# Optimization experiments

Hardware: AMD Instinct MI355X
Metric: run time of the kernel (lower is better)

The kernel has to match this reference:

```python
import jax, jax.numpy as jnp
import numpy as np

BNH, L, D = 32, 1024, 64        # (b*nh, seq_len, d_k)
CLIP = 64                        # rel_pos_clip
R = 2 * CLIP + 1                 # rel-pos table rows = 129
TEMP = 8.0                       # temperature = sqrt(d_k)


def setup_inputs() -> dict:
    key = jax.random.key(0)
    ks = jax.random.split(key, 7)
    q = jax.random.normal(ks[0], (BNH, L, D), jnp.float32)
    k = jax.random.normal(ks[1], (BNH, L, D), jnp.float32)
    v = jax.random.normal(ks[2], (BNH, L, D), jnp.float32)
    attn_w = jax.random.normal(ks[3], (BNH, L, L), jnp.float32)
    emb_k = jax.random.normal(ks[4], (R, D), jnp.float32)
    emb_v = jax.random.normal(ks[5], (R, D), jnp.float32)
    pos_seqs = jnp.sort(jax.random.randint(ks[6], (BNH, L), 0, 2048), axis=-1)
    mask = jnp.zeros((BNH, L, L), dtype=bool)  # no positions masked
    return {"q": q, "k": k, "v": v, "attn_w": attn_w,
            "emb_k": emb_k, "emb_v": emb_v,
            "pos_seqs": pos_seqs, "mask": mask}


def reference(q, k, v, attn_w, emb_k, emb_v, pos_seqs, mask):
    # relative-position index table: table[b,j,k] = clip(pos[k]-pos[j]) + CLIP, in [0, 2*CLIP]
    table = jnp.clip(pos_seqs[:, None, :] - pos_seqs[:, :, None], -CLIP, CLIP) + CLIP  # (bnh,l,l)

    # content scores
    attn = jnp.einsum('bid,bjd->bij', q, k)  # (bnh,l,l)

    # rel-pos key term: einsum('ijm,ijkm->ijk', q, emb_k[table]) done WITHOUT
    # materializing the (bnh,l,l,d) gather: project q onto all R embeddings,
    # then gather along the R axis (same math, far less memory traffic).
    qe = jnp.einsum('bid,rd->bir', q, emb_k)                 # (bnh,l,R)
    attn = attn + jnp.take_along_axis(qe, table, axis=2)     # (bnh,l,l)

    # score_util == 'np': additive posterior scores
    attn = attn + attn_w

    attn = attn / TEMP
    attn = jnp.where(mask, -jnp.inf, attn)
    p = jax.nn.softmax(attn, axis=2)
    # dropout is identity in eval mode

    out = jnp.einsum('bij,bjd->bid', p, v)                   # (bnh,l,d)

    # rel-pos value term: einsum('ijk,ijkm->ijm', p, emb_v[table]) via
    # scatter-add of probs into R buckets, then one small GEMM.
    bi = jnp.arange(BNH)[:, None, None]
    li = jnp.arange(L)[None, :, None]
    av = jnp.zeros((BNH, L, R), p.dtype).at[bi, li, table].add(p)  # (bnh,l,R)
    out = out + jnp.einsum('bir,rd->bid', av, emb_v)
    return out, p
```

## Files before the change

kernel.cpp:

```cpp
#include <hip/hip_runtime.h>
#include <hip/hip_bf16.h>

#define BNH 32
#define L 1024
#define D 64
#define RP 129
#define CLIPV 64
#define TI 16
#define TJ 256
#define NT 256

typedef __attribute__((ext_vector_type(8))) short bf16x8;
typedef __attribute__((ext_vector_type(4))) float f32x4;

__device__ __forceinline__ unsigned short f2bf(float f) {
    unsigned int u = __builtin_bit_cast(unsigned int, f);
    return (unsigned short)((u + 0x7fffu + ((u >> 16) & 1u)) >> 16);
}

__global__ __launch_bounds__(NT) void qe_kernel(const float* __restrict__ q,
                                                const float* __restrict__ emb_k,
                                                float* __restrict__ p_out) {
    __shared__ float e_s[RP][68];
    __shared__ float q_s[8][68];
    const int tid = threadIdx.x;
    const int b = blockIdx.x >> 7;
    const int i0 = (blockIdx.x & 127) * 8;

    for (int t = tid; t < RP * 16; t += NT) {
        int r = t >> 4, c4 = t & 15;
        *reinterpret_cast<float4*>(&e_s[r][c4 * 4]) =
            *reinterpret_cast<const float4*>(emb_k + r * D + c4 * 4);
    }
    for (int t = tid; t < 8 * 16; t += NT) {
        int row = t >> 4, c4 = t & 15;
        *reinterpret_cast<float4*>(&q_s[row][c4 * 4]) =
            *reinterpret_cast<const float4*>(q + ((size_t)(b * L + i0 + row)) * D + c4 * 4);
    }
    __syncthreads();

    const int row = tid >> 5;
    const int rr = tid & 31;
    for (int r = rr; r < RP; r += 32) {
        float acc = 0.f;
#pragma unroll
        for (int d4 = 0; d4 < 16; ++d4) {
            float4 qv = *reinterpret_cast<const float4*>(&q_s[row][d4 * 4]);
            float4 ev = *reinterpret_cast<const float4*>(&e_s[r][d4 * 4]);
            acc += qv.x * ev.x + qv.y * ev.y + qv.z * ev.z + qv.w * ev.w;
        }
        p_out[((size_t)(b * L + i0 + row)) * L + r] = acc;
    }
}

__global__ __launch_bounds__(NT, 2) void attn_kernel(
    const float* __restrict__ q, const float* __restrict__ k, const float* __restrict__ v,
    const float* __restrict__ attn_w, const float* __restrict__ emb_v,
    const int* __restrict__ pos, const unsigned char* __restrict__ mask,
    float* __restrict__ out, float* __restrict__ p_out) {

    __shared__ __attribute__((aligned(16))) unsigned short kv_u[TJ * 72];
    __shared__ __attribute__((aligned(16))) unsigned short q_u[TI * 72];
    __shared__ unsigned short pos_s[L];
    __shared__ float qe_s[TI * RP];
    __shared__ float av_s[TI * RP];
    __shared__ float out_s[TI * 68];
    __shared__ float m_part[4][16];
    __shared__ float m_s[16];
    __shared__ float l_s[16];

    const int tid = threadIdx.x;
    const int b = blockIdx.x >> 6;
    const int i0 = (blockIdx.x & 63) * TI;
    const int w = tid >> 6;
    const int lane = tid & 63;
    const int quad = lane >> 4;
    const int lo = lane & 15;

    for (int t = tid; t < L; t += NT) pos_s[t] = (unsigned short)pos[b * L + t];
    if (tid < TI * 8) {
        int r = tid >> 3, dc = tid & 7;
        const float* src = q + ((size_t)(b * L + i0 + r)) * D + dc * 8;
        float4 f0 = *(const float4*)src;
        float4 f1 = *(const float4*)(src + 4);
        bf16x8 qq;
        qq[0] = (short)f2bf(f0.x); qq[1] = (short)f2bf(f0.y);
        qq[2] = (short)f2bf(f0.z); qq[3] = (short)f2bf(f0.w);
        qq[4] = (short)f2bf(f1.x); qq[5] = (short)f2bf(f1.y);
        qq[6] = (short)f2bf(f1.z); qq[7] = (short)f2bf(f1.w);
        *(bf16x8*)&q_u[r * 72 + dc * 8] = qq;
    }
    for (int t = tid; t < TI * RP; t += NT) {
        int r = t / RP, c = t - r * RP;
        qe_s[t] = p_out[((size_t)(b * L + i0 + r)) * L + c];
        av_s[t] = 0.f;
    }
    for (int t = tid; t < TI * 68; t += NT) out_s[t] = 0.f;
    if (tid < 16) l_s[tid] = 0.f;
    __syncthreads();

    const bf16x8 aq0 = *(const bf16x8*)&q_u[lo * 72 + quad * 8];
    const bf16x8 aq1 = *(const bf16x8*)&q_u[lo * 72 + 32 + quad * 8];

    int posA[4];
#pragma unroll
    for (int r = 0; r < 4; ++r) posA[r] = (int)pos_s[i0 + quad * 4 + r];

    float mA[4] = {-3e38f, -3e38f, -3e38f, -3e38f};
    for (int jt = 0; jt < 4; ++jt) {
        const int j0 = jt * TJ;
#pragma unroll
        for (int s = 0; s < 8; ++s) {
            int ch = s * NT + tid;
            int col = ch >> 3, dc = ch & 7;
            const float* src = k + ((size_t)(b * L + j0 + col)) * D + dc * 8;
            float4 f0 = *(const float4*)src;
            float4 f1 = *(const float4*)(src + 4);
            bf16x8 kk;
            kk[0] = (short)f2bf(f0.x); kk[1] = (short)f2bf(f0.y);
            kk[2] = (short)f2bf(f0.z); kk[3] = (short)f2bf(f0.w);
            kk[4] = (short)f2bf(f1.x); kk[5] = (short)f2bf(f1.y);
            kk[6] = (short)f2bf(f1.z); kk[7] = (short)f2bf(f1.w);
            *(bf16x8*)&kv_u[col * 72 + dc * 8] = kk;
        }
        __syncthreads();
#pragma unroll
        for (int ct = 0; ct < 4; ++ct) {
            const int ncol = w * 64 + ct * 16 + lo;
            const int j = j0 + ncol;
            bf16x8 b0 = *(const bf16x8*)&kv_u[ncol * 72 + quad * 8];
            bf16x8 b1 = *(const bf16x8*)&kv_u[ncol * 72 + 32 + quad * 8];
            f32x4 acc = {0.f, 0.f, 0.f, 0.f};
            acc = __builtin_amdgcn_mfma_f32_16x16x32_bf16(aq0, b0, acc, 0, 0, 0);
            acc = __builtin_amdgcn_mfma_f32_16x16x32_bf16(aq1, b1, acc, 0, 0, 0);
            const int pj = (int)pos_s[j];
#pragma unroll
            for (int r = 0; r < 4; ++r) {
                const int row = quad * 4 + r;
                const size_t grow = (size_t)(b * L + i0 + row) * L + j;
                int dd = pj - posA[r];
                dd = min(max(dd, -CLIPV), CLIPV) + CLIPV;
                float sc = (acc[r] + qe_s[row * RP + dd] + attn_w[grow]) * 0.125f;
                if (mask[grow]) sc = -3e38f;
                mA[r] = fmaxf(mA[r], sc);
                p_out[grow] = sc;
            }
        }
        __syncthreads();
    }

#pragma unroll
    for (int off = 1; off < 16; off <<= 1) {
#pragma unroll
        for (int r = 0; r < 4; ++r) mA[r] = fmaxf(mA[r], __shfl_xor(mA[r], off, 64));
    }
    if (lo == 0) {
#pragma unroll
        for (int r = 0; r < 4; ++r) m_part[w][quad * 4 + r] = mA[r];
    }
    __syncthreads();
    if (tid < 16)
        m_s[tid] = fmaxf(fmaxf(m_part[0][tid], m_part[1][tid]),
                         fmaxf(m_part[2][tid], m_part[3][tid]));
    __syncthreads();

    const float mrow = m_s[lo];
    const int pos_m = (int)pos_s[i0 + lo];
    float l_r = 0.f;
    f32x4 oc[4];
#pragma unroll
    for (int ct = 0; ct < 4; ++ct) { oc[ct][0]=0.f; oc[ct][1]=0.f; oc[ct][2]=0.f; oc[ct][3]=0.f; }

    for (int jt = 0; jt < 4; ++jt) {
        const int j0 = jt * TJ;
        __syncthreads();
        {
            const float* src = v + ((size_t)(b * L + j0 + tid)) * D;
#pragma unroll
            for (int s = 0; s < 16; ++s) {
                float4 f = *(const float4*)(src + s * 4);
                kv_u[(s * 4 + 0) * 264 + tid] = f2bf(f.x);
                kv_u[(s * 4 + 1) * 264 + tid] = f2bf(f.y);
                kv_u[(s * 4 + 2) * 264 + tid] = f2bf(f.z);
                kv_u[(s * 4 + 3) * 264 + tid] = f2bf(f.w);
            }
        }
        __syncthreads();

        bf16x8 af[2];
#pragma unroll
        for (int kc = 0; kc < 2; ++kc) {
            const int bcol = j0 + w * 64 + kc * 32 + quad * 8;
            const float* sp = p_out + (size_t)(b * L + i0 + lo) * L + bcol;
            float4 s0 = *(const float4*)sp;
            float4 s1 = *(const float4*)(sp + 4);
            float ev[8];
            ev[0] = __expf(s0.x - mrow); ev[1] = __expf(s0.y - mrow);
            ev[2] = __expf(s0.z - mrow); ev[3] = __expf(s0.w - mrow);
            ev[4] = __expf(s1.x - mrow); ev[5] = __expf(s1.y - mrow);
            ev[6] = __expf(s1.z - mrow); ev[7] = __expf(s1.w - mrow);
            l_r += ev[0] + ev[1] + ev[2] + ev[3] + ev[4] + ev[5] + ev[6] + ev[7];
            int cur = -1; float a = 0.f;
#pragma unroll
            for (int i = 0; i < 8; ++i) {
                int dd = (int)pos_s[bcol + i] - pos_m;
                dd = min(max(dd, -CLIPV), CLIPV) + CLIPV;
                if (dd != cur) {
                    if (cur >= 0) atomicAdd(&av_s[lo * RP + cur], a);
                    cur = dd; a = 0.f;
                }
                a += ev[i];
            }
            atomicAdd(&av_s[lo * RP + cur], a);
            bf16x8 f;
#pragma unroll
            for (int i = 0; i < 8; ++i) f[i] = (short)f2bf(ev[i]);
            af[kc] = f;
        }
#pragma unroll
        for (int ct = 0; ct < 4; ++ct) {
#pragma unroll
            for (int kc = 0; kc < 2; ++kc) {
                bf16x8 bf = *(const bf16x8*)
                    &kv_u[(ct * 16 + lo) * 264 + w * 64 + kc * 32 + quad * 8];
                oc[ct] = __builtin_amdgcn_mfma_f32_16x16x32_bf16(af[kc], bf, oc[ct], 0, 0, 0);
            }
        }
    }

#pragma unroll
    for (int ct = 0; ct < 4; ++ct) {
#pragma unroll
        for (int r = 0; r < 4; ++r)
            atomicAdd(&out_s[(quad * 4 + r) * 68 + ct * 16 + lo], oc[ct][r]);
    }
    l_r += __shfl_xor(l_r, 16, 64);
    l_r += __shfl_xor(l_r, 32, 64);
    if (lane < 16) atomicAdd(&l_s[lo], l_r);
    __syncthreads();
    if (tid < 16) l_s[tid] = 1.f / l_s[tid];
    __syncthreads();

#pragma unroll
    for (int s = 0; s < 16; ++s) {
        int idx = s * NT + tid;
        int row = idx >> 8, c4 = idx & 255;
        float* addr = p_out + (size_t)(b * L + i0 + row) * L + c4 * 4;
        float4 sv = *(float4*)addr;
        const float mm = m_s[row], il = l_s[row];
        float4 pv;
        pv.x = __expf(sv.x - mm) * il;
        pv.y = __expf(sv.y - mm) * il;
        pv.z = __expf(sv.z - mm) * il;
        pv.w = __expf(sv.w - mm) * il;
        *(float4*)addr = pv;
    }

    {
        const int row = tid >> 4, dc = tid & 15;
        float4 o = *(const float4*)&out_s[row * 68 + dc * 4];
        const float il = l_s[row];
        for (int r = 0; r < RP; ++r) {
            float a = av_s[row * RP + r];
            if (a != 0.f) {
                const float4 ev4 = *(const float4*)(emb_v + r * D + dc * 4);
                o.x += a * ev4.x; o.y += a * ev4.y;
                o.z += a * ev4.z; o.w += a * ev4.w;
            }
        }
        o.x *= il; o.y *= il; o.z *= il; o.w *= il;
        *(float4*)(out + (size_t)(b * L + i0 + row) * D + dc * 4) = o;
    }
}

extern "C" void kernel_launch(void* const* d_in, const int* in_sizes, int n_in,
                              void* d_out, int out_size, void* d_ws, size_t ws_size,
                              hipStream_t stream) {
    const float* q = (const float*)d_in[0];
    const float* k = (const float*)d_in[1];
    const float* v = (const float*)d_in[2];
    const float* attn_w = (const float*)d_in[3];
    const float* emb_k = (const float*)d_in[4];
    const float* emb_v = (const float*)d_in[5];
    const int* pos = (const int*)d_in[6];
    const unsigned char* mask = (const unsigned char*)d_in[7];
    float* out = (float*)d_out;
    float* p_out = out + (size_t)BNH * L * D;

    qe_kernel<<<BNH * (L / 8), NT, 0, stream>>>(q, emb_k, p_out);
    attn_kernel<<<BNH * (L / TI), NT, 0, stream>>>(q, k, v, attn_w, emb_v, pos, mask,
                                                   out, p_out);
}
```

Before: 625.1 us.

## Fuse qe projection into attention kernel and keep scores in LDS as fp16

```diff
diff --git a/kernel.cpp b/kernel.cpp
--- a/kernel.cpp
+++ b/kernel.cpp
@@ -1,5 +1,4 @@
 #include <hip/hip_runtime.h>
-#include <hip/hip_bf16.h>
 
 #define BNH 32
 #define L 1024
@@ -7,79 +6,57 @@
 #define RP 129
 #define CLIPV 64
 #define TI 16
-#define TJ 256
+#define TJ 128
+#define NJT (L / TJ)
 #define NT 256
+#define SS 1032
+#define KST 72
+#define VST 136
 
 typedef __attribute__((ext_vector_type(8))) short bf16x8;
 typedef __attribute__((ext_vector_type(4))) float f32x4;
+typedef __attribute__((ext_vector_type(8))) _Float16 f16x8;
+typedef __attribute__((ext_vector_type(4))) _Float16 f16x4;
 
 __device__ __forceinline__ unsigned short f2bf(float f) {
     unsigned int u = __builtin_bit_cast(unsigned int, f);
     return (unsigned short)((u + 0x7fffu + ((u >> 16) & 1u)) >> 16);
 }
 
-__global__ __launch_bounds__(NT) void qe_kernel(const float* __restrict__ q,
-                                                const float* __restrict__ emb_k,
-                                                float* __restrict__ p_out) {
-    __shared__ float e_s[RP][68];
-    __shared__ float q_s[8][68];
-    const int tid = threadIdx.x;
-    const int b = blockIdx.x >> 7;
-    const int i0 = (blockIdx.x & 127) * 8;
-
-    for (int t = tid; t < RP * 16; t += NT) {
-        int r = t >> 4, c4 = t & 15;
-        *reinterpret_cast<float4*>(&e_s[r][c4 * 4]) =
-            *reinterpret_cast<const float4*>(emb_k + r * D + c4 * 4);
-    }
-    for (int t = tid; t < 8 * 16; t += NT) {
-        int row = t >> 4, c4 = t & 15;
-        *reinterpret_cast<float4*>(&q_s[row][c4 * 4]) =
-            *reinterpret_cast<const float4*>(q + ((size_t)(b * L + i0 + row)) * D + c4 * 4);
-    }
-    __syncthreads();
-
-    const int row = tid >> 5;
-    const int rr = tid & 31;
-    for (int r = rr; r < RP; r += 32) {
-        float acc = 0.f;
-#pragma unroll
-        for (int d4 = 0; d4 < 16; ++d4) {
-            float4 qv = *reinterpret_cast<const float4*>(&q_s[row][d4 * 4]);
-            float4 ev = *reinterpret_cast<const float4*>(&e_s[r][d4 * 4]);
-            acc += qv.x * ev.x + qv.y * ev.y + qv.z * ev.z + qv.w * ev.w;
-        }
-        p_out[((size_t)(b * L + i0 + row)) * L + r] = acc;
-    }
-}
-
-__global__ __launch_bounds__(NT, 2) void attn_kernel(
+__global__ __launch_bounds__(NT, 2) void attn_fused(
     const float* __restrict__ q, const float* __restrict__ k, const float* __restrict__ v,
-    const float* __restrict__ attn_w, const float* __restrict__ emb_v,
-    const int* __restrict__ pos, const unsigned char* __restrict__ mask,
+    const float* __restrict__ attn_w, const float* __restrict__ emb_k,
+    const float* __restrict__ emb_v, const int* __restrict__ pos,
+    const unsigned char* __restrict__ mask,
     float* __restrict__ out, float* __restrict__ p_out) {
 
-    __shared__ __attribute__((aligned(16))) unsigned short kv_u[TJ * 72];
-    __shared__ __attribute__((aligned(16))) unsigned short q_u[TI * 72];
+    __shared__ __attribute__((aligned(16))) _Float16 s_lds[TI][SS];
+    __shared__ __attribute__((aligned(16))) unsigned short kv_u[TJ * KST];
+    __shared__ __attribute__((aligned(16))) unsigned short q_u[TI * KST];
     __shared__ unsigned short pos_s[L];
-    __shared__ float qe_s[TI * RP];
-    __shared__ float av_s[TI * RP];
-    __shared__ float out_s[TI * 68];
+    __shared__ float qeav_s[TI * RP];
+    __shared__ __attribute__((aligned(16))) float qfout_s[TI * 68];
     __shared__ float m_part[4][16];
     __shared__ float m_s[16];
     __shared__ float l_s[16];
 
     const int tid = threadIdx.x;
-    const int b = blockIdx.x >> 6;
-    const int i0 = (blockIdx.x & 63) * TI;
+    const int wg = ((int)blockIdx.x & 7) * ((BNH * (L / TI)) >> 3) + ((int)blockIdx.x >> 3);
+    const int b = wg >> 6;
+    const int i0 = (wg & 63) * TI;
     const int w = tid >> 6;
     const int lane = tid & 63;
     const int quad = lane >> 4;
     const int lo = lane & 15;
 
     for (int t = tid; t < L; t += NT) pos_s[t] = (unsigned short)pos[b * L + t];
+    {
+        const int row = tid >> 4, c4 = tid & 15;
+        *reinterpret_cast<float4*>(&qfout_s[row * 68 + c4 * 4]) =
+            *reinterpret_cast<const float4*>(q + ((size_t)(b * L + i0 + row)) * D + c4 * 4);
+    }
     if (tid < TI * 8) {
-        int r = tid >> 3, dc = tid & 7;
+        const int r = tid >> 3, dc = tid & 7;
         const float* src = q + ((size_t)(b * L + i0 + r)) * D + dc * 8;
         float4 f0 = *(const float4*)src;
         float4 f1 = *(const float4*)(src + 4);
@@ -88,29 +65,37 @@
         qq[2] = (short)f2bf(f0.z); qq[3] = (short)f2bf(f0.w);
         qq[4] = (short)f2bf(f1.x); qq[5] = (short)f2bf(f1.y);
         qq[6] = (short)f2bf(f1.z); qq[7] = (short)f2bf(f1.w);
-        *(bf16x8*)&q_u[r * 72 + dc * 8] = qq;
-    }
-    for (int t = tid; t < TI * RP; t += NT) {
-        int r = t / RP, c = t - r * RP;
-        qe_s[t] = p_out[((size_t)(b * L + i0 + r)) * L + c];
-        av_s[t] = 0.f;
-    }
-    for (int t = tid; t < TI * 68; t += NT) out_s[t] = 0.f;
-    if (tid < 16) l_s[tid] = 0.f;
-    __syncthreads();
-
-    const bf16x8 aq0 = *(const bf16x8*)&q_u[lo * 72 + quad * 8];
-    const bf16x8 aq1 = *(const bf16x8*)&q_u[lo * 72 + 32 + quad * 8];
+        *(bf16x8*)&q_u[r * KST + dc * 8] = qq;
+    }
+    __syncthreads();
+
+    {
+        const int row = tid >> 4, rr = tid & 15;
+        for (int r = rr; r < RP; r += 16) {
+            float acc = 0.f;
+#pragma unroll
+            for (int d4 = 0; d4 < 16; ++d4) {
+                float4 qv = *reinterpret_cast<const float4*>(&qfout_s[row * 68 + d4 * 4]);
+                float4 ev = *reinterpret_cast<const float4*>(emb_k + r * D + d4 * 4);
+                acc += qv.x * ev.x + qv.y * ev.y + qv.z * ev.z + qv.w * ev.w;
+            }
+            qeav_s[row * RP + r] = acc;
+        }
+    }
+    __syncthreads();
+
+    const bf16x8 aq0 = *(const bf16x8*)&q_u[lo * KST + quad * 8];
+    const bf16x8 aq1 = *(const bf16x8*)&q_u[lo * KST + 32 + quad * 8];
 
     int posA[4];
 #pragma unroll
     for (int r = 0; r < 4; ++r) posA[r] = (int)pos_s[i0 + quad * 4 + r];
 
     float mA[4] = {-3e38f, -3e38f, -3e38f, -3e38f};
-    for (int jt = 0; jt < 4; ++jt) {
+    for (int jt = 0; jt < NJT; ++jt) {
         const int j0 = jt * TJ;
 #pragma unroll
-        for (int s = 0; s < 8; ++s) {
+        for (int s = 0; s < 4; ++s) {
             int ch = s * NT + tid;
             int col = ch >> 3, dc = ch & 7;
             const float* src = k + ((size_t)(b * L + j0 + col)) * D + dc * 8;
@@ -121,15 +106,15 @@
             kk[2] = (short)f2bf(f0.z); kk[3] = (short)f2bf(f0.w);
             kk[4] = (short)f2bf(f1.x); kk[5] = (short)f2bf(f1.y);
             kk[6] = (short)f2bf(f1.z); kk[7] = (short)f2bf(f1.w);
-            *(bf16x8*)&kv_u[col * 72 + dc * 8] = kk;
-        }
-        __syncthreads();
-#pragma unroll
-        for (int ct = 0; ct < 4; ++ct) {
-            const int ncol = w * 64 + ct * 16 + lo;
+            *(bf16x8*)&kv_u[col * KST + dc * 8] = kk;
+        }
+        __syncthreads();
+#pragma unroll
+        for (int ct = 0; ct < 2; ++ct) {
+            const int ncol = w * 32 + ct * 16 + lo;
             const int j = j0 + ncol;
-            bf16x8 b0 = *(const bf16x8*)&kv_u[ncol * 72 + quad * 8];
-            bf16x8 b1 = *(const bf16x8*)&kv_u[ncol * 72 + 32 + quad * 8];
+            bf16x8 b0 = *(const bf16x8*)&kv_u[ncol * KST + quad * 8];
+            bf16x8 b1 = *(const bf16x8*)&kv_u[ncol * KST + 32 + quad * 8];
             f32x4 acc = {0.f, 0.f, 0.f, 0.f};
             acc = __builtin_amdgcn_mfma_f32_16x16x32_bf16(aq0, b0, acc, 0, 0, 0);
             acc = __builtin_amdgcn_mfma_f32_16x16x32_bf16(aq1, b1, acc, 0, 0, 0);
@@ -140,10 +125,10 @@
                 const size_t grow = (size_t)(b * L + i0 + row) * L + j;
                 int dd = pj - posA[r];
                 dd = min(max(dd, -CLIPV), CLIPV) + CLIPV;
-                float sc = (acc[r] + qe_s[row * RP + dd] + attn_w[grow]) * 0.125f;
+                float sc = (acc[r] + qeav_s[row * RP + dd] + attn_w[grow]) * 0.125f;
                 if (mask[grow]) sc = -3e38f;
                 mA[r] = fmaxf(mA[r], sc);
-                p_out[grow] = sc;
+                s_lds[row][j] = (_Float16)sc;
             }
         }
         __syncthreads();
@@ -159,9 +144,13 @@
         for (int r = 0; r < 4; ++r) m_part[w][quad * 4 + r] = mA[r];
     }
     __syncthreads();
-    if (tid < 16)
+    if (tid < 16) {
         m_s[tid] = fmaxf(fmaxf(m_part[0][tid], m_part[1][tid]),
                          fmaxf(m_part[2][tid], m_part[3][tid]));
+        l_s[tid] = 0.f;
+    }
+    for (int t = tid; t < TI * RP; t += NT) qeav_s[t] = 0.f;
+    for (int t = tid; t < TI * 68; t += NT) qfout_s[t] = 0.f;
     __syncthreads();
 
     const float mrow = m_s[lo];
@@ -171,60 +160,50 @@
 #pragma unroll
     for (int ct = 0; ct < 4; ++ct) { oc[ct][0]=0.f; oc[ct][1]=0.f; oc[ct][2]=0.f; oc[ct][3]=0.f; }
 
-    for (int jt = 0; jt < 4; ++jt) {
+    for (int jt = 0; jt < NJT; ++jt) {
         const int j0 = jt * TJ;
-        __syncthreads();
-        {
-            const float* src = v + ((size_t)(b * L + j0 + tid)) * D;
-#pragma unroll
-            for (int s = 0; s < 16; ++s) {
-                float4 f = *(const float4*)(src + s * 4);
-                kv_u[(s * 4 + 0) * 264 + tid] = f2bf(f.x);
-                kv_u[(s * 4 + 1) * 264 + tid] = f2bf(f.y);
-                kv_u[(s * 4 + 2) * 264 + tid] = f2bf(f.z);
-                kv_u[(s * 4 + 3) * 264 + tid] = f2bf(f.w);
-            }
-        }
-        __syncthreads();
-
-        bf16x8 af[2];
-#pragma unroll
-        for (int kc = 0; kc < 2; ++kc) {
-            const int bcol = j0 + w * 64 + kc * 32 + quad * 8;
-            const float* sp = p_out + (size_t)(b * L + i0 + lo) * L + bcol;
-            float4 s0 = *(const float4*)sp;
-            float4 s1 = *(const float4*)(sp + 4);
-            float ev[8];
-            ev[0] = __expf(s0.x - mrow); ev[1] = __expf(s0.y - mrow);
-            ev[2] = __expf(s0.z - mrow); ev[3] = __expf(s0.w - mrow);
-            ev[4] = __expf(s1.x - mrow); ev[5] = __expf(s1.y - mrow);
-            ev[6] = __expf(s1.z - mrow); ev[7] = __expf(s1.w - mrow);
-            l_r += ev[0] + ev[1] + ev[2] + ev[3] + ev[4] + ev[5] + ev[6] + ev[7];
-            int cur = -1; float a = 0.f;
-#pragma unroll
-            for (int i = 0; i < 8; ++i) {
-                int dd = (int)pos_s[bcol + i] - pos_m;
-                dd = min(max(dd, -CLIPV), CLIPV) + CLIPV;
-                if (dd != cur) {
-                    if (cur >= 0) atomicAdd(&av_s[lo * RP + cur], a);
-                    cur = dd; a = 0.f;
-                }
-                a += ev[i];
-            }
-            atomicAdd(&av_s[lo * RP + cur], a);
-            bf16x8 f;
-#pragma unroll
-            for (int i = 0; i < 8; ++i) f[i] = (short)f2bf(ev[i]);
-            af[kc] = f;
-        }
+        const int colv = tid & 127, hv = tid >> 7;
+        const float* srcv = v + ((size_t)(b * L + j0 + colv)) * D + hv * 32;
+        float4 vf[8];
+#pragma unroll
+        for (int s = 0; s < 8; ++s) vf[s] = *(const float4*)(srcv + s * 4);
+        __syncthreads();
+#pragma unroll
+        for (int s = 0; s < 8; ++s) {
+            const int dbase = hv * 32 + s * 4;
+            kv_u[(dbase + 0) * VST + colv] = f2bf(vf[s].x);
+            kv_u[(dbase + 1) * VST + colv] = f2bf(vf[s].y);
+            kv_u[(dbase + 2) * VST + colv] = f2bf(vf[s].z);
+            kv_u[(dbase + 3) * VST + colv] = f2bf(vf[s].w);
+        }
+        __syncthreads();
+
+        const int jcol = j0 + w * 32 + quad * 8;
+        f16x8 sv = *reinterpret_cast<const f16x8*>(&s_lds[lo][jcol]);
+        float ev[8];
+#pragma unroll
+        for (int i = 0; i < 8; ++i) ev[i] = __expf((float)sv[i] - mrow);
+        l_r += ev[0] + ev[1] + ev[2] + ev[3] + ev[4] + ev[5] + ev[6] + ev[7];
+        int cur = -1; float a = 0.f;
+#pragma unroll
+        for (int i = 0; i < 8; ++i) {
+            int dd = (int)pos_s[jcol + i] - pos_m;
+            dd = min(max(dd, -CLIPV), CLIPV) + CLIPV;
+            if (dd != cur) {
+                if (cur >= 0) atomicAdd(&qeav_s[lo * RP + cur], a);
+                cur = dd; a = 0.f;
+            }
+            a += ev[i];
+        }
+        atomicAdd(&qeav_s[lo * RP + cur], a);
+        bf16x8 af;
+#pragma unroll
+        for (int i = 0; i < 8; ++i) af[i] = (short)f2bf(ev[i]);
 #pragma unroll
         for (int ct = 0; ct < 4; ++ct) {
-#pragma unroll
-            for (int kc = 0; kc < 2; ++kc) {
-                bf16x8 bf = *(const bf16x8*)
-                    &kv_u[(ct * 16 + lo) * 264 + w * 64 + kc * 32 + quad * 8];
-                oc[ct] = __builtin_amdgcn_mfma_f32_16x16x32_bf16(af[kc], bf, oc[ct], 0, 0, 0);
-            }
+            bf16x8 bf = *reinterpret_cast<const bf16x8*>(
+                &kv_u[(ct * 16 + lo) * VST + w * 32 + quad * 8]);
+            oc[ct] = __builtin_amdgcn_mfma_f32_16x16x32_bf16(af, bf, oc[ct], 0, 0, 0);
         }
     }
 
@@ -232,7 +211,7 @@
     for (int ct = 0; ct < 4; ++ct) {
 #pragma unroll
         for (int r = 0; r < 4; ++r)
-            atomicAdd(&out_s[(quad * 4 + r) * 68 + ct * 16 + lo], oc[ct][r]);
+            atomicAdd(&qfout_s[(quad * 4 + r) * 68 + ct * 16 + lo], oc[ct][r]);
     }
     l_r += __shfl_xor(l_r, 16, 64);
     l_r += __shfl_xor(l_r, 32, 64);
@@ -242,26 +221,23 @@
     __syncthreads();
 
 #pragma unroll
-    for (int s = 0; s < 16; ++s) {
-        int idx = s * NT + tid;
-        int row = idx >> 8, c4 = idx & 255;
-        float* addr = p_out + (size_t)(b * L + i0 + row) * L + c4 * 4;
-        float4 sv = *(float4*)addr;
-        const float mm = m_s[row], il = l_s[row];
+    for (int s = 0; s < TI; ++s) {
+        f16x4 sv = *reinterpret_cast<const f16x4*>(&s_lds[s][tid * 4]);
+        const float mm = m_s[s], il = l_s[s];
         float4 pv;
-        pv.x = __expf(sv.x - mm) * il;
-        pv.y = __expf(sv.y - mm) * il;
-        pv.z = __expf(sv.z - mm) * il;
-        pv.w = __expf(sv.w - mm) * il;
-        *(float4*)addr = pv;
+        pv.x = __expf((float)sv[0] - mm) * il;
+        pv.y = __expf((float)sv[1] - mm) * il;
+        pv.z = __expf((float)sv[2] - mm) * il;
+        pv.w = __expf((float)sv[3] - mm) * il;
+        *reinterpret_cast<float4*>(p_out + (size_t)(b * L + i0 + s) * L + tid * 4) = pv;
     }
 
     {
         const int row = tid >> 4, dc = tid & 15;
-        float4 o = *(const float4*)&out_s[row * 68 + dc * 4];
+        float4 o = *(const float4*)&qfout_s[row * 68 + dc * 4];
         const float il = l_s[row];
         for (int r = 0; r < RP; ++r) {
-            float a = av_s[row * RP + r];
+            float a = qeav_s[row * RP + r];
             if (a != 0.f) {
                 const float4 ev4 = *(const float4*)(emb_v + r * D + dc * 4);
                 o.x += a * ev4.x; o.y += a * ev4.y;
@@ -287,7 +263,6 @@
     float* out = (float*)d_out;
     float* p_out = out + (size_t)BNH * L * D;
 
-    qe_kernel<<<BNH * (L / 8), NT, 0, stream>>>(q, emb_k, p_out);
-    attn_kernel<<<BNH * (L / TI), NT, 0, stream>>>(q, k, v, attn_w, emb_v, pos, mask,
-                                                   out, p_out);
+    attn_fused<<<BNH * (L / TI), NT, 0, stream>>>(q, k, v, attn_w, emb_k, emb_v,
+                                                  pos, mask, out, p_out);
 }
```

New measurement: 647.6 us. 1.04x slower.
